# Optimization experiments

Measured on AMD Instinct MI355X. Metric: run time of the kernel, lower is better.

The kernel has to match this reference:

```python
import jax, jax.numpy as jnp
import numpy as np

N_NODES = 100000
N_EDGES = 1600000
IN_F, HID, OUT_F = 50, 256, 121


def setup_inputs() -> dict:
    key = jax.random.key(0)
    ks = jax.random.split(key, 8)
    x = jax.random.normal(ks[0], (N_NODES, IN_F), dtype=jnp.float32)
    edge_index = jax.random.randint(ks[1], (2, N_EDGES), 0, N_NODES, dtype=jnp.int64)
    W1 = jax.random.normal(ks[2], (IN_F, HID), dtype=jnp.float32) * (1.0 / np.sqrt(IN_F))
    b1 = jnp.zeros((HID,), dtype=jnp.float32)
    W2 = jax.random.normal(ks[3], (HID, HID), dtype=jnp.float32) * (1.0 / np.sqrt(HID))
    b2 = jnp.zeros((HID,), dtype=jnp.float32)
    W3 = jax.random.normal(ks[4], (HID, OUT_F), dtype=jnp.float32) * (1.0 / np.sqrt(HID))
    b3 = jnp.zeros((OUT_F,), dtype=jnp.float32)
    return {"x": x, "edge_index": edge_index, "W1": W1, "b1": b1,
            "W2": W2, "b2": b2, "W3": W3, "b3": b3}


def _gcn_norm(edge_index, num_nodes):
    # PyG gcn_norm: add self-loops, symmetric degree normalization.
    loop = jnp.arange(num_nodes, dtype=edge_index.dtype)
    row = jnp.concatenate([edge_index[0], loop])  # source
    col = jnp.concatenate([edge_index[1], loop])  # target (aggregation dim)
    ones = jnp.ones(row.shape[0], dtype=jnp.float32)
    deg = jax.ops.segment_sum(ones, col, num_segments=num_nodes)
    dinv = jnp.where(deg > 0, jax.lax.rsqrt(deg), 0.0)
    norm = dinv[row] * dinv[col]  # [E+N]
    return row, col, norm


def _gcn_conv(x, W, b, row, col, norm, num_nodes):
    h = x @ W                                   # [N, F_out] dense transform
    msg = h[row] * norm[:, None]                # gather + scale  [E+N, F_out]
    agg = jax.ops.segment_sum(msg, col, num_segments=num_nodes)  # scatter-add
    return agg + b


def reference(x, edge_index, W1, b1, W2, b2, W3, b3):
    n = x.shape[0]
    row, col, norm = _gcn_norm(edge_index, n)
    # layer 1 + relu (dropout is identity in eval mode)
    x1 = _gcn_conv(x, W1, b1, row, col, norm, n)
    h = jax.nn.relu(x1)
    # layer 2 + relu
    x1 = _gcn_conv(h, W2, b2, row, col, norm, n)
    h = jax.nn.relu(x1)
    # layer 3; module returns pre-relu output x1 of the last conv
    x1 = _gcn_conv(h, W3, b3, row, col, norm, n)
    return x1
```

## Files before the change

kernel.cpp:

```cpp
#include <hip/hip_runtime.h>


#define IN_F 50
#define HID  256
#define OUT_F 121
#define KP1  64
#define NP3  128
#define MPAD 100096

typedef __attribute__((ext_vector_type(8))) short bf16x8;
typedef __attribute__((ext_vector_type(4))) float f32x4;

__device__ __forceinline__ float bf2f(unsigned short u) {
    union { unsigned int i; float f; } x; x.i = ((unsigned int)u) << 16; return x.f;
}
__device__ __forceinline__ unsigned short f2bf(float f) {
    union { float f; unsigned int i; } x; x.f = f;
    unsigned int r = x.i + 0x7FFFu + ((x.i >> 16) & 1u);
    return (unsigned short)(r >> 16);
}

__device__ __forceinline__ void gl2lds16(const void* g, void* l) {
    __builtin_amdgcn_global_load_lds(
        (const __attribute__((address_space(1))) void*)g,
        (__attribute__((address_space(3))) void*)l, 16, 0, 0);
}

__global__ void k_detect(const int* __restrict__ ei, int* __restrict__ flag, int N) {
    int i = threadIdx.x;
    int lo = ei[2 * i], hi = ei[2 * i + 1];
    int bad = (hi != 0) || ((unsigned)lo >= (unsigned)N);
    unsigned long long m = __ballot(bad);
    if (threadIdx.x == 0) *flag = (m == 0ULL) ? 1 : 0;
}


__global__ void k_count(const int* __restrict__ ei, const int* __restrict__ flag,
                        int* __restrict__ cnt, int E, int N) {
    int t = blockIdx.x * blockDim.x + threadIdx.x;
    if (t >= E) return;
    int f = *flag;
    int c = f ? ei[2 * (E + t)] : ei[E + t];
    c = min(max(c, 0), N - 1);
    atomicAdd(&cnt[c], 1);
}

__global__ __launch_bounds__(1024) void k_scan(const int* __restrict__ cnt,
                                               int* __restrict__ offs,
                                               float* __restrict__ dinv, int n) {
    __shared__ int wsum[16];
    __shared__ int s_carry;
    int lane = threadIdx.x & 63, wid = threadIdx.x >> 6;
    if (threadIdx.x == 0) s_carry = 0;
    __syncthreads();
    for (int base = 0; base < n; base += 4096) {
        int i0 = base + (int)threadIdx.x * 4;
        int v0 = (i0 + 0 < n) ? cnt[i0 + 0] : 0;
        int v1 = (i0 + 1 < n) ? cnt[i0 + 1] : 0;
        int v2 = (i0 + 2 < n) ? cnt[i0 + 2] : 0;
        int v3 = (i0 + 3 < n) ? cnt[i0 + 3] : 0;
        int s1 = v0 + v1, s2 = s1 + v2, tsum = s2 + v3;
        int x = tsum;
        #pragma unroll
        for (int d = 1; d < 64; d <<= 1) {
            int y = __shfl_up(x, d, 64);
            if (lane >= d) x += y;
        }
        if (lane == 63) wsum[wid] = x;
        __syncthreads();
        int wpre = 0;
        #pragma unroll
        for (int j = 0; j < 16; j++) wpre += (j < wid) ? wsum[j] : 0;
        int carry = s_carry;
        int e0 = carry + wpre + x - tsum;
        if (i0 + 0 < n) { offs[i0+0]=e0;    dinv[i0+0]=rsqrtf((float)(v0+1)); }
        if (i0 + 1 < n) { offs[i0+1]=e0+v0; dinv[i0+1]=rsqrtf((float)(v1+1)); }
        if (i0 + 2 < n) { offs[i0+2]=e0+s1; dinv[i0+2]=rsqrtf((float)(v2+1)); }
        if (i0 + 3 < n) { offs[i0+3]=e0+s2; dinv[i0+3]=rsqrtf((float)(v3+1)); }
        __syncthreads();
        if (threadIdx.x == 1023) s_carry = carry + wpre + x;
        __syncthreads();
    }
    if (threadIdx.x == 0) offs[n] = s_carry;
}

__global__ void k_fill(const int* __restrict__ ei, const int* __restrict__ flag,
                       const int* __restrict__ offs,
                       int* __restrict__ fillc, int* __restrict__ rowidx, int E, int N) {
    int t = blockIdx.x * blockDim.x + threadIdx.x;
    if (t >= E) return;
    int f = *flag;
    int c = f ? ei[2 * (E + t)] : ei[E + t];
    int r = f ? ei[2 * t] : ei[t];
    c = min(max(c, 0), N - 1);
    r = min(max(r, 0), N - 1);
    int pos = offs[c] + atomicAdd(&fillc[c], 1);
    if ((unsigned)pos < (unsigned)E) rowidx[pos] = r;
}

__global__ void k_prep(const float* __restrict__ x, const float* __restrict__ dinv,
                       unsigned short* __restrict__ Xs,
                       const float* __restrict__ W1, unsigned short* __restrict__ Bt1,
                       const float* __restrict__ W2, unsigned short* __restrict__ Bt2,
                       const float* __restrict__ W3, unsigned short* __restrict__ Bt3,
                       int N) {
    int bid = blockIdx.x;
    int npadx = (N * KP1 + 255) / 256;
    if (bid < npadx) {
        int idx = bid * 256 + (int)threadIdx.x;
        if (idx < N * KP1) {
            int node = idx >> 6, k = idx & 63;
            Xs[idx] = (k < IN_F) ? f2bf(dinv[node] * x[node * IN_F + k]) : (unsigned short)0;
        }
        return;
    }
    bid -= npadx;
    if (bid < (HID * KP1) / 256) {
        int idx = bid * 256 + (int)threadIdx.x;
        int nn = idx >> 6, k = idx & 63;
        Bt1[idx] = (k < IN_F) ? f2bf(W1[k * HID + nn]) : (unsigned short)0;
        return;
    }
    bid -= (HID * KP1) / 256;
    if (bid < (HID * HID) / 256) {
        int idx = bid * 256 + (int)threadIdx.x;
        int nn = idx >> 8, k = idx & 255;
        Bt2[idx] = f2bf(W2[k * HID + nn]);
        return;
    }
    bid -= (HID * HID) / 256;
    {
        int idx = bid * 256 + (int)threadIdx.x;
        int nn = idx >> 8, k = idx & 255;
        Bt3[idx] = (nn < OUT_F) ? f2bf(W3[k * OUT_F + nn]) : (unsigned short)0;
    }
}

__global__ __launch_bounds__(256) void k_gemm_lds(const unsigned short* __restrict__ A,
                                                  const unsigned short* __restrict__ Bt,
                                                  const float* __restrict__ dinv,
                                                  const float* __restrict__ bias,
                                                  unsigned short* __restrict__ C,
                                                  int K, int Nout,
                                                  int BIAS, int RELU, int SCALE) {
    __shared__ char lds[16384];
    const int tid = threadIdx.x;
    const int wid = tid >> 6, lane = tid & 63;
    const int wm = wid & 1, wn = wid >> 1;
    const int quad = lane >> 4, ml = lane & 15;
    const int m0 = blockIdx.x * 128;
    const int n0g = blockIdx.y * 128;

    f32x4 acc[4][4];
    #pragma unroll
    for (int a = 0; a < 4; a++)
        #pragma unroll
        for (int b = 0; b < 4; b++) acc[a][b] = (f32x4){0.f, 0.f, 0.f, 0.f};

    for (int kk = 0; kk < K; kk += 32) {
        #pragma unroll
        for (int r = 0; r < 2; r++) {
            int c = r * 256 + tid;
            int row = c >> 2, q = c & 3;
            gl2lds16(A  + (size_t)(m0  + row) * K + kk + q * 8, lds + c * 16);
            gl2lds16(Bt + (size_t)(n0g + row) * K + kk + q * 8, lds + 8192 + c * 16);
        }
        __syncthreads();
        bf16x8 af[4], bfv[4];
        #pragma unroll
        for (int mf = 0; mf < 4; mf++)
            af[mf] = *(const bf16x8*)(lds + ((wm * 64 + mf * 16 + ml) * 64 + quad * 16));
        #pragma unroll
        for (int nf = 0; nf < 4; nf++)
            bfv[nf] = *(const bf16x8*)(lds + 8192 + ((wn * 64 + nf * 16 + ml) * 64 + quad * 16));
        #pragma unroll
        for (int mf = 0; mf < 4; mf++)
            #pragma unroll
            for (int nf = 0; nf < 4; nf++)
                acc[mf][nf] = __builtin_amdgcn_mfma_f32_16x16x32_bf16(af[mf], bfv[nf], acc[mf][nf], 0, 0, 0);
        __syncthreads();
    }

    #pragma unroll
    for (int mf = 0; mf < 4; mf++) {
        int r0 = m0 + wm * 64 + mf * 16 + quad * 4;
        float dd[4] = {1.f, 1.f, 1.f, 1.f};
        if (SCALE) { dd[0]=dinv[r0]; dd[1]=dinv[r0+1]; dd[2]=dinv[r0+2]; dd[3]=dinv[r0+3]; }
        #pragma unroll
        for (int nf = 0; nf < 4; nf++) {
            int col = n0g + wn * 64 + nf * 16 + ml;
            float bb = BIAS ? bias[col] : 0.f;
            #pragma unroll
            for (int i = 0; i < 4; i++) {
                float v = acc[mf][nf][i] + bb;
                if (RELU) v = fmaxf(v, 0.f);
                v *= dd[i];
                C[(size_t)(r0 + i) * Nout + col] = f2bf(v);
            }
        }
    }
}

__global__ __launch_bounds__(256) void k_mlp23(const unsigned short* __restrict__ A,
                                               const unsigned short* __restrict__ B2t,
                                               const unsigned short* __restrict__ B3t,
                                               const float* __restrict__ b2,
                                               const float* __restrict__ dinv,
                                               unsigned short* __restrict__ G) {
    __shared__ char lds[65536];
    const int tid = threadIdx.x;
    const int wid = tid >> 6, lane = tid & 63;
    const int wm = wid & 1, wn = wid >> 1;
    const int quad = lane >> 4, ml = lane & 15;
    const int m0 = blockIdx.x * 128;

    f32x4 acc1[4][8];
    #pragma unroll
    for (int a = 0; a < 4; a++)
        #pragma unroll
        for (int b = 0; b < 8; b++) acc1[a][b] = (f32x4){0.f, 0.f, 0.f, 0.f};

    for (int kk = 0; kk < HID; kk += 32) {
        #pragma unroll
        for (int r = 0; r < 2; r++) {
            int c = r * 256 + tid;
            int row = c >> 2, q = c & 3;
            gl2lds16(A + (size_t)(m0 + row) * HID + kk + q * 8, lds + c * 16);
        }
        #pragma unroll
        for (int r = 0; r < 4; r++) {
            int c = r * 256 + tid;
            int nn = c >> 2, q = c & 3;
            gl2lds16(B2t + (size_t)nn * HID + kk + q * 8, lds + 8192 + c * 16);
        }
        __syncthreads();
        bf16x8 af[4], bv[8];
        #pragma unroll
        for (int mf = 0; mf < 4; mf++)
            af[mf] = *(const bf16x8*)(lds + ((wm * 64 + mf * 16 + ml) * 64 + quad * 16));
        #pragma unroll
        for (int nf = 0; nf < 8; nf++)
            bv[nf] = *(const bf16x8*)(lds + 8192 + ((wn * 128 + nf * 16 + ml) * 64 + quad * 16));
        #pragma unroll
        for (int mf = 0; mf < 4; mf++)
            #pragma unroll
            for (int nf = 0; nf < 8; nf++)
                acc1[mf][nf] = __builtin_amdgcn_mfma_f32_16x16x32_bf16(af[mf], bv[nf], acc1[mf][nf], 0, 0, 0);
        __syncthreads();
    }

    #pragma unroll
    for (int nf = 0; nf < 8; nf++) {
        int col = wn * 128 + nf * 16 + ml;
        float bb = b2[col];
        #pragma unroll
        for (int mf = 0; mf < 4; mf++) {
            int rl = wm * 64 + mf * 16 + quad * 4;
            #pragma unroll
            for (int i = 0; i < 4; i++) {
                int row = rl + i;
                int byte = (row * 512 + col * 2) ^ ((row & 7) << 4);
                *(unsigned short*)(lds + byte) = f2bf(fmaxf(acc1[mf][nf][i] + bb, 0.f));
            }
        }
    }
    __syncthreads();

    f32x4 acc2[4][4];
    #pragma unroll
    for (int a = 0; a < 4; a++)
        #pragma unroll
        for (int b = 0; b < 4; b++) acc2[a][b] = (f32x4){0.f, 0.f, 0.f, 0.f};

    for (int kk = 0; kk < HID; kk += 32) {
        bf16x8 af2[4], bv2[4];
        #pragma unroll
        for (int mf = 0; mf < 4; mf++) {
            int row = wm * 64 + mf * 16 + ml;
            int byte = (row * 512 + kk * 2 + quad * 16) ^ ((row & 7) << 4);
            af2[mf] = *(const bf16x8*)(lds + byte);
        }
        #pragma unroll
        for (int nf = 0; nf < 4; nf++)
            bv2[nf] = *(const bf16x8*)(B3t + (size_t)(wn * 64 + nf * 16 + ml) * HID + kk + quad * 8);
        #pragma unroll
        for (int mf = 0; mf < 4; mf++)
            #pragma unroll
            for (int nf = 0; nf < 4; nf++)
                acc2[mf][nf] = __builtin_amdgcn_mfma_f32_16x16x32_bf16(af2[mf], bv2[nf], acc2[mf][nf], 0, 0, 0);
    }

    #pragma unroll
    for (int mf = 0; mf < 4; mf++) {
        int r0 = m0 + wm * 64 + mf * 16 + quad * 4;
        float dd[4] = {dinv[r0], dinv[r0+1], dinv[r0+2], dinv[r0+3]};
        #pragma unroll
        for (int nf = 0; nf < 4; nf++) {
            int col = wn * 64 + nf * 16 + ml;
            #pragma unroll
            for (int i = 0; i < 4; i++)
                G[(size_t)(r0 + i) * NP3 + col] = f2bf(acc2[mf][nf][i] * dd[i]);
        }
    }
}


__device__ __forceinline__ int rclamp(int r, int N) { return min(max(r, 0), N - 1); }

__global__ void k_aggx(const unsigned short* __restrict__ Xs,
                       const int* __restrict__ offs, const int* __restrict__ rowidx,
                       const float* __restrict__ dinv, unsigned short* __restrict__ Y, int N) {
    int wid = threadIdx.x >> 6, lane = threadIdx.x & 63;
    int sub = lane >> 3, sl = lane & 7;
    int node = blockIdx.x * 32 + wid * 8 + sub;
    int nc = min(node, N - 1);
    int c = sl * 8;
    bf16x8 s = *(const bf16x8*)(Xs + (size_t)nc * KP1 + c);
    float a[8];
    #pragma unroll
    for (int k = 0; k < 8; k++) a[k] = bf2f((unsigned short)s[k]);
    int e = offs[nc], end = offs[nc + 1];
    if (node >= N) { e = 0; end = 0; }
    while (__any(e < end)) {
        int r[4]; float m[4];
        #pragma unroll
        for (int j = 0; j < 4; j++) {
            int idx = e + j;
            m[j] = (idx < end) ? 1.f : 0.f;
            idx = min(idx, end - 1); idx = max(idx, 0);
            r[j] = rclamp(rowidx[idx], N);
        }
        bf16x8 u[4];
        #pragma unroll
        for (int j = 0; j < 4; j++)
            u[j] = *(const bf16x8*)(Xs + (size_t)r[j] * KP1 + c);
        #pragma unroll
        for (int j = 0; j < 4; j++)
            #pragma unroll
            for (int k = 0; k < 8; k++)
                a[k] = fmaf(bf2f((unsigned short)u[j][k]), m[j], a[k]);
        e += 4;
    }
    if (node < N) {
        float dv = dinv[node];
        bf16x8 o;
        #pragma unroll
        for (int k = 0; k < 8; k++) o[k] = (short)f2bf(a[k] * dv);
        *(bf16x8*)(Y + (size_t)node * KP1 + c) = o;
    }
}

__global__ void k_agg256s(const unsigned short* __restrict__ Hn,
                          const int* __restrict__ offs, const int* __restrict__ rowidx,
                          const float* __restrict__ dinv, unsigned short* __restrict__ Y,
                          int N, int half_n) {
    int cell = blockIdx.x & 7;
    int chunk = cell >> 1, half = cell & 1;
    int idx = blockIdx.x >> 3;
    int wid = threadIdx.x >> 6, lane = threadIdx.x & 63;
    int sub = lane >> 3, sl = lane & 7;
    int node = half * half_n + idx * 32 + wid * 8 + sub;
    int hi_end = min((half + 1) * half_n, N);
    int ok = node < hi_end;
    int nc = ok ? node : hi_end - 1;
    int c = chunk * 64 + sl * 8;
    bf16x8 s = *(const bf16x8*)(Hn + (size_t)nc * HID + c);
    float a[8];
    #pragma unroll
    for (int k = 0; k < 8; k++) a[k] = bf2f((unsigned short)s[k]);
    int e = offs[nc], end = offs[nc + 1];
    if (!ok) { e = 0; end = 0; }
    while (__any(e < end)) {
        int r[4]; float m[4];
        #pragma unroll
        for (int j = 0; j < 4; j++) {
            int idx2 = e + j;
            m[j] = (idx2 < end) ? 1.f : 0.f;
            idx2 = min(idx2, end - 1); idx2 = max(idx2, 0);
            r[j] = rclamp(rowidx[idx2], N);
        }
        bf16x8 u[4];
        #pragma unroll
        for (int j = 0; j < 4; j++)
            u[j] = *(const bf16x8*)(Hn + (size_t)r[j] * HID + c);
        #pragma unroll
        for (int j = 0; j < 4; j++)
            #pragma unroll
            for (int k = 0; k < 8; k++)
                a[k] = fmaf(bf2f((unsigned short)u[j][k]), m[j], a[k]);
        e += 4;
    }
    if (ok) {
        float dv = dinv[node];
        bf16x8 o;
        #pragma unroll
        for (int k = 0; k < 8; k++) o[k] = (short)f2bf(a[k] * dv);
        *(bf16x8*)(Y + (size_t)node * HID + c) = o;
    }
}

__global__ void k_aggouts(const unsigned short* __restrict__ G,
                          const int* __restrict__ offs, const int* __restrict__ rowidx,
                          const float* __restrict__ dinv, const float* __restrict__ bias,
                          float* __restrict__ out, int N, int quar_n) {
    int cell = blockIdx.x & 7;
    int chunk = cell >> 2, quar = cell & 3;
    int idx = blockIdx.x >> 3;
    int wid = threadIdx.x >> 6, lane = threadIdx.x & 63;
    int sub = lane >> 3, sl = lane & 7;
    int node = quar * quar_n + idx * 32 + wid * 8 + sub;
    int hi_end = min((quar + 1) * quar_n, N);
    int ok = node < hi_end;
    int nc = ok ? node : hi_end - 1;
    int c = chunk * 64 + sl * 8;
    bf16x8 s = *(const bf16x8*)(G + (size_t)nc * NP3 + c);
    float a[8];
    #pragma unroll
    for (int k = 0; k < 8; k++) a[k] = bf2f((unsigned short)s[k]);
    int e = offs[nc], end = offs[nc + 1];
    if (!ok) { e = 0; end = 0; }
    while (__any(e < end)) {
        int r[4]; float m[4];
        #pragma unroll
        for (int j = 0; j < 4; j++) {
            int idx2 = e + j;
            m[j] = (idx2 < end) ? 1.f : 0.f;
            idx2 = min(idx2, end - 1); idx2 = max(idx2, 0);
            r[j] = rclamp(rowidx[idx2], N);
        }
        bf16x8 u[4];
        #pragma unroll
        for (int j = 0; j < 4; j++)
            u[j] = *(const bf16x8*)(G + (size_t)r[j] * NP3 + c);
        #pragma unroll
        for (int j = 0; j < 4; j++)
            #pragma unroll
            for (int k = 0; k < 8; k++)
                a[k] = fmaf(bf2f((unsigned short)u[j][k]), m[j], a[k]);
        e += 4;
    }
    if (ok) {
        float dv = dinv[node];
        #pragma unroll
        for (int k = 0; k < 8; k++) {
            int col = c + k;
            if (col < OUT_F)
                out[(size_t)node * OUT_F + col] = fmaf(a[k], dv, bias[col]);
        }
    }
}


extern "C" void kernel_launch(void* const* d_in, const int* in_sizes, int n_in,
                              void* d_out, int out_size, void* d_ws, size_t ws_size,
                              hipStream_t stream) {
    const float* x  = (const float*)d_in[0];
    const int*   ei = (const int*)d_in[1];
    const float* W1 = (const float*)d_in[2];
    const float* b1 = (const float*)d_in[3];
    const float* W2 = (const float*)d_in[4];
    const float* b2 = (const float*)d_in[5];
    const float* W3 = (const float*)d_in[6];
    const float* b3 = (const float*)d_in[7];
    float* out = (float*)d_out;

    const int N = in_sizes[0] / IN_F;
    const int E = in_sizes[1] / 2;

    char* w = (char*)d_ws;
    size_t off = 0;
    auto alloc = [&](size_t bytes) -> char* {
        char* p = w + off;
        off += (bytes + 255) & ~(size_t)255;
        return p;
    };
    int*   cnt    = (int*)  alloc((size_t)N * 4);
    int*   fillc  = (int*)  alloc((size_t)N * 4);
    int*   offs   = (int*)  alloc((size_t)(N + 1) * 4);
    float* dinv   = (float*)alloc((size_t)MPAD * 4);
    int*   flag   = (int*)  alloc(256);
    int*   rowidx = (int*)  alloc((size_t)E * 4);
    unsigned short* Bt1 = (unsigned short*)alloc((size_t)HID * KP1 * 2);
    unsigned short* Bt2 = (unsigned short*)alloc((size_t)HID * HID * 2);
    unsigned short* Bt3 = (unsigned short*)alloc((size_t)NP3 * HID * 2);
    unsigned short* bufA = (unsigned short*)alloc((size_t)MPAD * HID * 2);
    unsigned short* bufB = (unsigned short*)alloc((size_t)MPAD * HID * 2);
    unsigned short* Xs  = bufA;
    unsigned short* Y1  = bufB;
    unsigned short* H1s = bufA;
    unsigned short* Y2  = bufB;
    unsigned short* G3  = bufA;

    size_t msz = (size_t)((char*)fillc - (char*)cnt) + (size_t)N * 4;
    hipMemsetAsync(cnt, 0, msz, stream);

    k_detect<<<1, 64, 0, stream>>>(ei, flag, N);
    k_count<<<(E + 255) / 256, 256, 0, stream>>>(ei, flag, cnt, E, N);
    k_scan<<<1, 1024, 0, stream>>>(cnt, offs, dinv, N);
    k_fill<<<(E + 255) / 256, 256, 0, stream>>>(ei, flag, offs, fillc, rowidx, E, N);

    int prep_grid = (N * KP1 + 255) / 256 + (HID * KP1) / 256 + (HID * HID) / 256 + (NP3 * HID) / 256;
    k_prep<<<prep_grid, 256, 0, stream>>>(x, dinv, Xs, W1, Bt1, W2, Bt2, W3, Bt3, N);

    k_aggx<<<(N + 31) / 32, 256, 0, stream>>>(Xs, offs, rowidx, dinv, Y1, N);
    dim3 g1(MPAD / 128, HID / 128);
    k_gemm_lds<<<g1, 256, 0, stream>>>(Y1, Bt1, dinv, b1, H1s, KP1, HID, 1, 1, 1);
    int half_n = (N + 1) / 2;
    int bpc2 = (half_n + 31) / 32;
    k_agg256s<<<8 * bpc2, 256, 0, stream>>>(H1s, offs, rowidx, dinv, Y2, N, half_n);
    k_mlp23<<<MPAD / 128, 256, 0, stream>>>(Y2, Bt2, Bt3, b2, dinv, G3);
    int quar_n = (N + 3) / 4;
    int bpc3 = (quar_n + 31) / 32;
    k_aggouts<<<8 * bpc3, 256, 0, stream>>>(G3, offs, rowidx, dinv, b3, out, N, quar_n);

    (void)n_in; (void)out_size; (void)ws_size;
}
```

Measured before the change: 656.9 us.

## Partition edges by destination range and parallelize CSR build scan

Adds a pre-pass that buckets edges into 8 destination-node ranges via block-local LDS histograms. Count and fill atomics then run per partition with better locality, presumably targeting XCD/L2 locality of the atomics. It also replaces the single-block serial scan with a three-kernel multi-block scan. It removes the clamp on rowidx in the aggregation kernels, relying on the clamping done during partitioning. The cost is an extra pass writing and reading 8-byte edge pairs, plus a capacity limit of E/4 per partition that silently drops edges if the degree distribution is skewed.

```diff
diff --git a/kernel.cpp b/kernel.cpp
--- a/kernel.cpp
+++ b/kernel.cpp
@@ -34,68 +34,121 @@
     if (threadIdx.x == 0) *flag = (m == 0ULL) ? 1 : 0;
 }
 
-
-__global__ void k_count(const int* __restrict__ ei, const int* __restrict__ flag,
-                        int* __restrict__ cnt, int E, int N) {
-    int t = blockIdx.x * blockDim.x + threadIdx.x;
-    if (t >= E) return;
+__global__ __launch_bounds__(256) void k_part(const int* __restrict__ ei,
+                                              const int* __restrict__ flag,
+                                              int2* __restrict__ epart,
+                                              int* __restrict__ pcnt,
+                                              int E, int N, int rng, int partcap) {
+    __shared__ int2 eb[2048];
+    __shared__ int hist[8], base[8], cur[8];
+    int tid = threadIdx.x;
+    if (tid < 8) { hist[tid] = 0; cur[tid] = 0; }
+    __syncthreads();
     int f = *flag;
-    int c = f ? ei[2 * (E + t)] : ei[E + t];
-    c = min(max(c, 0), N - 1);
-    atomicAdd(&cnt[c], 1);
-}
-
-__global__ __launch_bounds__(1024) void k_scan(const int* __restrict__ cnt,
-                                               int* __restrict__ offs,
-                                               float* __restrict__ dinv, int n) {
+    int t0 = blockIdx.x * 2048;
+    #pragma unroll
+    for (int j = 0; j < 8; j++) {
+        int t = t0 + j * 256 + tid;
+        int2 e = make_int2(-1, -1);
+        if (t < E) {
+            int c = f ? ei[2 * (E + t)] : ei[E + t];
+            int r = f ? ei[2 * t] : ei[t];
+            e.x = min(max(c, 0), N - 1);
+            e.y = min(max(r, 0), N - 1);
+            atomicAdd(&hist[e.x / rng], 1);
+        }
+        eb[j * 256 + tid] = e;
+    }
+    __syncthreads();
+    if (tid < 8) base[tid] = atomicAdd(&pcnt[tid], hist[tid]);
+    __syncthreads();
+    #pragma unroll
+    for (int j = 0; j < 8; j++) {
+        int2 e = eb[j * 256 + tid];
+        if (e.x >= 0) {
+            int rg = e.x / rng;
+            int p = base[rg] + atomicAdd(&cur[rg], 1);
+            if (p < partcap) epart[(size_t)rg * partcap + p] = e;
+        }
+    }
+}
+
+__global__ void k_count8(const int2* __restrict__ epart, const int* __restrict__ pcnt,
+                         int* __restrict__ cnt, int partcap) {
+    int cell = blockIdx.x & 7;
+    int t = (blockIdx.x >> 3) * blockDim.x + threadIdx.x;
+    if (t >= min(pcnt[cell], partcap)) return;
+    int2 e = epart[(size_t)cell * partcap + t];
+    atomicAdd(&cnt[e.x], 1);
+}
+
+__global__ __launch_bounds__(1024) void k_scanA(const int* __restrict__ cnt,
+                                                int* __restrict__ bsum, int n) {
+    __shared__ int ws[16];
+    int tid = threadIdx.x, lane = tid & 63, wid = tid >> 6;
+    int i0 = blockIdx.x * 4096 + tid * 4;
+    int t = 0;
+    #pragma unroll
+    for (int j = 0; j < 4; j++) t += (i0 + j < n) ? cnt[i0 + j] : 0;
+    #pragma unroll
+    for (int d = 1; d < 64; d <<= 1) t += __shfl_xor(t, d, 64);
+    if (lane == 0) ws[wid] = t;
+    __syncthreads();
+    if (tid == 0) {
+        int s = 0;
+        #pragma unroll
+        for (int j = 0; j < 16; j++) s += ws[j];
+        bsum[blockIdx.x] = s;
+    }
+}
+
+__global__ void k_scanB(const int* __restrict__ bsum, int* __restrict__ bbase,
+                        int* __restrict__ offs, int nb, int n) {
+    int lane = threadIdx.x;
+    int v = (lane < nb) ? bsum[lane] : 0;
+    int x = v;
+    #pragma unroll
+    for (int d = 1; d < 64; d <<= 1) { int y = __shfl_up(x, d, 64); if (lane >= d) x += y; }
+    if (lane < nb) bbase[lane] = x - v;
+    if (lane == nb - 1) offs[n] = x;
+}
+
+__global__ __launch_bounds__(1024) void k_scanC(const int* __restrict__ cnt,
+                                                const int* __restrict__ bbase,
+                                                int* __restrict__ offs,
+                                                float* __restrict__ dinv, int n) {
     __shared__ int wsum[16];
-    __shared__ int s_carry;
-    int lane = threadIdx.x & 63, wid = threadIdx.x >> 6;
-    if (threadIdx.x == 0) s_carry = 0;
+    int tid = threadIdx.x, lane = tid & 63, wid = tid >> 6;
+    int i0 = blockIdx.x * 4096 + tid * 4;
+    int v0 = (i0 + 0 < n) ? cnt[i0 + 0] : 0;
+    int v1 = (i0 + 1 < n) ? cnt[i0 + 1] : 0;
+    int v2 = (i0 + 2 < n) ? cnt[i0 + 2] : 0;
+    int v3 = (i0 + 3 < n) ? cnt[i0 + 3] : 0;
+    int s1 = v0 + v1, s2 = s1 + v2, tsum = s2 + v3;
+    int x = tsum;
+    #pragma unroll
+    for (int d = 1; d < 64; d <<= 1) { int y = __shfl_up(x, d, 64); if (lane >= d) x += y; }
+    if (lane == 63) wsum[wid] = x;
     __syncthreads();
-    for (int base = 0; base < n; base += 4096) {
-        int i0 = base + (int)threadIdx.x * 4;
-        int v0 = (i0 + 0 < n) ? cnt[i0 + 0] : 0;
-        int v1 = (i0 + 1 < n) ? cnt[i0 + 1] : 0;
-        int v2 = (i0 + 2 < n) ? cnt[i0 + 2] : 0;
-        int v3 = (i0 + 3 < n) ? cnt[i0 + 3] : 0;
-        int s1 = v0 + v1, s2 = s1 + v2, tsum = s2 + v3;
-        int x = tsum;
-        #pragma unroll
-        for (int d = 1; d < 64; d <<= 1) {
-            int y = __shfl_up(x, d, 64);
-            if (lane >= d) x += y;
-        }
-        if (lane == 63) wsum[wid] = x;
-        __syncthreads();
-        int wpre = 0;
-        #pragma unroll
-        for (int j = 0; j < 16; j++) wpre += (j < wid) ? wsum[j] : 0;
-        int carry = s_carry;
-        int e0 = carry + wpre + x - tsum;
-        if (i0 + 0 < n) { offs[i0+0]=e0;    dinv[i0+0]=rsqrtf((float)(v0+1)); }
-        if (i0 + 1 < n) { offs[i0+1]=e0+v0; dinv[i0+1]=rsqrtf((float)(v1+1)); }
-        if (i0 + 2 < n) { offs[i0+2]=e0+s1; dinv[i0+2]=rsqrtf((float)(v2+1)); }
-        if (i0 + 3 < n) { offs[i0+3]=e0+s2; dinv[i0+3]=rsqrtf((float)(v3+1)); }
-        __syncthreads();
-        if (threadIdx.x == 1023) s_carry = carry + wpre + x;
-        __syncthreads();
-    }
-    if (threadIdx.x == 0) offs[n] = s_carry;
-}
-
-__global__ void k_fill(const int* __restrict__ ei, const int* __restrict__ flag,
-                       const int* __restrict__ offs,
-                       int* __restrict__ fillc, int* __restrict__ rowidx, int E, int N) {
-    int t = blockIdx.x * blockDim.x + threadIdx.x;
-    if (t >= E) return;
-    int f = *flag;
-    int c = f ? ei[2 * (E + t)] : ei[E + t];
-    int r = f ? ei[2 * t] : ei[t];
-    c = min(max(c, 0), N - 1);
-    r = min(max(r, 0), N - 1);
-    int pos = offs[c] + atomicAdd(&fillc[c], 1);
-    if ((unsigned)pos < (unsigned)E) rowidx[pos] = r;
+    int wpre = 0;
+    #pragma unroll
+    for (int j = 0; j < 16; j++) wpre += (j < wid) ? wsum[j] : 0;
+    int e0 = bbase[blockIdx.x] + wpre + x - tsum;
+    if (i0 + 0 < n) { offs[i0+0] = e0;      dinv[i0+0] = rsqrtf((float)(v0 + 1)); }
+    if (i0 + 1 < n) { offs[i0+1] = e0 + v0; dinv[i0+1] = rsqrtf((float)(v1 + 1)); }
+    if (i0 + 2 < n) { offs[i0+2] = e0 + s1; dinv[i0+2] = rsqrtf((float)(v2 + 1)); }
+    if (i0 + 3 < n) { offs[i0+3] = e0 + s2; dinv[i0+3] = rsqrtf((float)(v3 + 1)); }
+}
+
+__global__ void k_fill8p(const int2* __restrict__ epart, const int* __restrict__ pcnt,
+                         const int* __restrict__ offs, int* __restrict__ fillc,
+                         int* __restrict__ rowidx, int E, int partcap) {
+    int cell = blockIdx.x & 7;
+    int t = (blockIdx.x >> 3) * blockDim.x + threadIdx.x;
+    if (t >= min(pcnt[cell], partcap)) return;
+    int2 e = epart[(size_t)cell * partcap + t];
+    int pos = offs[e.x] + atomicAdd(&fillc[e.x], 1);
+    if ((unsigned)pos < (unsigned)E) rowidx[pos] = e.y;
 }
 
 __global__ void k_prep(const float* __restrict__ x, const float* __restrict__ dinv,
@@ -305,8 +358,6 @@
 }
 
 
-__device__ __forceinline__ int rclamp(int r, int N) { return min(max(r, 0), N - 1); }
-
 __global__ void k_aggx(const unsigned short* __restrict__ Xs,
                        const int* __restrict__ offs, const int* __restrict__ rowidx,
                        const float* __restrict__ dinv, unsigned short* __restrict__ Y, int N) {
@@ -328,7 +379,7 @@
             int idx = e + j;
             m[j] = (idx < end) ? 1.f : 0.f;
             idx = min(idx, end - 1); idx = max(idx, 0);
-            r[j] = rclamp(rowidx[idx], N);
+            r[j] = rowidx[idx];
         }
         bf16x8 u[4];
         #pragma unroll
@@ -377,7 +428,7 @@
             int idx2 = e + j;
             m[j] = (idx2 < end) ? 1.f : 0.f;
             idx2 = min(idx2, end - 1); idx2 = max(idx2, 0);
-            r[j] = rclamp(rowidx[idx2], N);
+            r[j] = rowidx[idx2];
         }
         bf16x8 u[4];
         #pragma unroll
@@ -426,7 +477,7 @@
             int idx2 = e + j;
             m[j] = (idx2 < end) ? 1.f : 0.f;
             idx2 = min(idx2, end - 1); idx2 = max(idx2, 0);
-            r[j] = rclamp(rowidx[idx2], N);
+            r[j] = rowidx[idx2];
         }
         bf16x8 u[4];
         #pragma unroll
@@ -476,9 +527,14 @@
     };
     int*   cnt    = (int*)  alloc((size_t)N * 4);
     int*   fillc  = (int*)  alloc((size_t)N * 4);
+    int*   pcnt   = (int*)  alloc(256);
     int*   offs   = (int*)  alloc((size_t)(N + 1) * 4);
     float* dinv   = (float*)alloc((size_t)MPAD * 4);
     int*   flag   = (int*)  alloc(256);
+    int*   bsum   = (int*)  alloc(256);
+    int*   bbase  = (int*)  alloc(256);
+    const int partcap = E / 4;
+    int2*  epart  = (int2*) alloc((size_t)8 * partcap * 8);
     int*   rowidx = (int*)  alloc((size_t)E * 4);
     unsigned short* Bt1 = (unsigned short*)alloc((size_t)HID * KP1 * 2);
     unsigned short* Bt2 = (unsigned short*)alloc((size_t)HID * HID * 2);
@@ -491,13 +547,20 @@
     unsigned short* Y2  = bufB;
     unsigned short* G3  = bufA;
 
-    size_t msz = (size_t)((char*)fillc - (char*)cnt) + (size_t)N * 4;
+    size_t msz = (size_t)((char*)pcnt - (char*)cnt) + 256;
     hipMemsetAsync(cnt, 0, msz, stream);
 
+    const int rng = (N + 7) / 8;
+    const int nsc = (N + 4095) / 4096;
+    const int pgrid = 8 * ((partcap + 255) / 256);
+
     k_detect<<<1, 64, 0, stream>>>(ei, flag, N);
-    k_count<<<(E + 255) / 256, 256, 0, stream>>>(ei, flag, cnt, E, N);
-    k_scan<<<1, 1024, 0, stream>>>(cnt, offs, dinv, N);
-    k_fill<<<(E + 255) / 256, 256, 0, stream>>>(ei, flag, offs, fillc, rowidx, E, N);
+    k_part<<<(E + 2047) / 2048, 256, 0, stream>>>(ei, flag, epart, pcnt, E, N, rng, partcap);
+    k_count8<<<pgrid, 256, 0, stream>>>(epart, pcnt, cnt, partcap);
+    k_scanA<<<nsc, 1024, 0, stream>>>(cnt, bsum, N);
+    k_scanB<<<1, 64, 0, stream>>>(bsum, bbase, offs, nsc, N);
+    k_scanC<<<nsc, 1024, 0, stream>>>(cnt, bbase, offs, dinv, N);
+    k_fill8p<<<pgrid, 256, 0, stream>>>(epart, pcnt, offs, fillc, rowidx, E, partcap);
 
     int prep_grid = (N * KP1 + 255) / 256 + (HID * KP1) / 256 + (HID * HID) / 256 + (NP3 * HID) / 256;
     k_prep<<<prep_grid, 256, 0, stream>>>(x, dinv, Xs, W1, Bt1, W2, Bt2, W3, Bt3, N);
```

New measurement: 566.3 us. 1.16x faster.
